# Performance work log

Measured on AMD Instinct MI355X. Metric: run time of the kernel, lower is better.

Reference implementation:

```python
import jax, jax.numpy as jnp
import numpy as np

N_PULSES = 8_000_000
NUM_DOMS = 200_000
EPS = 1e-08


def setup_inputs() -> dict:
    key = jax.random.key(0)
    k1, k2, k3 = jax.random.split(key, 3)
    times = jax.random.normal(k1, (N_PULSES,), dtype=jnp.float32) * 100.0
    charges = jax.random.uniform(k2, (N_PULSES,), dtype=jnp.float32) * 10.0
    dom_idx = jax.random.randint(k3, (N_PULSES,), 0, NUM_DOMS, dtype=jnp.int32)
    return {"times": times, "charges": charges, "dom_idx": dom_idx, "num_doms": NUM_DOMS}


def reference(times, charges, dom_idx, num_doms):
    n = times.shape[0]
    ones = jnp.ones_like(times)
    # per-DOM pulse counts (float, matching torch's float scatter_add of ones)
    count = jnp.zeros((num_doms,), dtype=times.dtype).at[dom_idx].add(ones)

    # --- temporal features ---
    first_times = jnp.full((num_doms,), jnp.inf, dtype=times.dtype).at[dom_idx].min(times)
    delta_t_first = times - first_times[dom_idx]

    mean_times = jnp.zeros((num_doms,), dtype=times.dtype).at[dom_idx].add(times) / (count + EPS)
    mean_e = mean_times[dom_idx]
    delta_t_median = times - mean_e

    var = jnp.zeros((num_doms,), dtype=times.dtype).at[dom_idx].add((times - mean_e) ** 2) / (count + EPS)
    time_std = jnp.sqrt(var + EPS)
    t_normalized = (times - mean_e) / (time_std[dom_idx] + EPS)

    # --- charge features ---
    total_charges = jnp.zeros((num_doms,), dtype=charges.dtype).at[dom_idx].add(charges)
    charge_fraction = charges / (total_charges[dom_idx] + EPS)

    max_charges = jnp.full((num_doms,), -jnp.inf, dtype=charges.dtype).at[dom_idx].max(charges)
    charge_ratio = charges / (max_charges[dom_idx] + EPS)

    # --- charge rank within each DOM (0 = brightest), fully vectorized ---
    # sort primarily by dom_idx, secondarily by descending charge
    order = jnp.lexsort((-charges, dom_idx))  # (n,)
    sorted_dom = dom_idx[order]
    counts_i = jnp.zeros((num_doms,), dtype=jnp.int32).at[dom_idx].add(jnp.ones_like(dom_idx))
    starts = jnp.cumsum(counts_i) - counts_i  # exclusive prefix-sum of group sizes
    rank_sorted = jnp.arange(n, dtype=jnp.int32) - starts[sorted_dom]
    ranks = jnp.zeros((n,), dtype=jnp.int32).at[order].set(rank_sorted)

    dom_sizes_e = count[dom_idx]  # float sizes per pulse
    log_charge_rank = jnp.log((ranks.astype(times.dtype) + 1.0) / (dom_sizes_e + EPS))

    return jnp.stack(
        [delta_t_first, delta_t_median, t_normalized,
         charge_fraction, charge_ratio, log_charge_rank], axis=1)
```

## Files before the change

### kernel.cpp

```cpp
#include <hip/hip_runtime.h>
#include <hip/hip_bf16.h>
#include <stdint.h>
#include <math.h>

#define NDOMS 200000
#define EPSF 1e-8f
#define DLBITS 8
#define DLMASK 255
#define NBUCK ((NDOMS + DLMASK) >> DLBITS)
#define NB2 (NBUCK * 2)
#define CAP_B 11264
#define CAP_H 6016
#define CSTRIDE 16
#define CHUNK 8192
#define IDXM 0x7FFFFFu

typedef unsigned long long u64;

__device__ __forceinline__ unsigned f2mono(float f){
  unsigned b = __float_as_uint(f);
  return b ^ (unsigned)(((int)b >> 31) | 0x80000000);
}
__device__ __forceinline__ float mono2f(unsigned u){
  unsigned b = (u & 0x80000000u) ? (u ^ 0x80000000u) : ~u;
  return __uint_as_float(b);
}

__global__ void k_init(int* __restrict__ gcursor){
  int i = blockIdx.x * blockDim.x + threadIdx.x;
  if (i < NB2) gcursor[i * CSTRIDE] = 0;
}

__global__ void __launch_bounds__(512)
k_bin(const float* __restrict__ charges, const int* __restrict__ dom,
      const float* __restrict__ times, int n, int* __restrict__ gcursor,
      uint4* __restrict__ rec_g){
  __shared__ int lhist[NB2];
  __shared__ int lbase[NB2];
  __shared__ int lcnt[NB2];
  int t = threadIdx.x;
  int start = blockIdx.x * CHUNK;
  int end = min(start + CHUNK, n);
  for (int i = t; i < NB2; i += 512) lhist[i] = 0;
  __syncthreads();
  for (int p = start + t; p < end; p += 512)
    atomicAdd(&lhist[dom[p] >> 7], 1);
  __syncthreads();
  for (int i = t; i < NB2; i += 512){
    int c = lhist[i];
    lbase[i] = c ? atomicAdd(&gcursor[i * CSTRIDE], c) : 0;
    lcnt[i] = 0;
  }
  __syncthreads();
  for (int p = start + t; p < end; p += 512){
    int d = dom[p];
    int i2 = d >> 7;
    int pos = lbase[i2] + atomicAdd(&lcnt[i2], 1);
    if (pos < CAP_B){
      int b = i2 >> 1;
      int slot = (i2 & 1) ? (CAP_B - 1 - pos) : pos;
      uint4 r;
      r.x = ((unsigned)(d & DLMASK) << 23) | (IDXM - (unsigned)p);
      r.y = __float_as_uint(charges[p]);
      r.z = __float_as_uint(times[p]);
      r.w = (unsigned)d;
      rec_g[(size_t)b * CAP_B + slot] = r;
    }
  }
}

__global__ void __launch_bounds__(512)
k_grp(const uint4* __restrict__ rec_g, const int* __restrict__ gcursor,
      float* __restrict__ derived, unsigned char* __restrict__ rank8p){
  __shared__ u64   keysL[CAP_H];
  __shared__ int hist[128], starts[128], cur[128];
  __shared__ float s_t[128], s_t2[128], s_c[128];
  __shared__ unsigned mn_t[128], mx_c[128];
  int bid = blockIdx.x, b = bid >> 1, h = bid & 1, t = threadIdx.x;
  int cl = min(gcursor[(2 * b) * CSTRIDE], CAP_B);
  int ch = min(gcursor[(2 * b + 1) * CSTRIDE], CAP_B - cl);
  int myCnt  = h ? ch : cl;
  if (myCnt > CAP_H) myCnt = CAP_H;
  int myBase = h ? (CAP_B - ch) : 0;
  const uint4* rg = rec_g + (size_t)b * CAP_B + myBase;

  if (t < 128){
    hist[t] = 0; s_t[t] = 0.f; s_t2[t] = 0.f; s_c[t] = 0.f;
    mn_t[t] = 0xFFFFFFFFu; mx_c[t] = 0u;
  }
  __syncthreads();
  unsigned rx[12], ry[12], rz[12];
  #pragma unroll
  for (int i = 0; i < 12; ++i){
    int s = t + i * 512;
    if (s < myCnt){
      uint4 r = rg[s];
      rx[i] = r.x; ry[i] = r.y; rz[i] = r.z;
      int dl = (int)((r.x >> 23) & 127);
      float tv = __uint_as_float(r.z);
      atomicAdd(&hist[dl], 1);
      atomicAdd(&s_t[dl], tv);
      atomicAdd(&s_t2[dl], tv * tv);
      atomicAdd(&s_c[dl], __uint_as_float(r.y));
      atomicMax(&mx_c[dl], r.y);
      atomicMin(&mn_t[dl], f2mono(tv));
    }
  }
  __syncthreads();
  if (t < 128) starts[t] = hist[t];
  __syncthreads();
  for (int off = 1; off < 128; off <<= 1){
    int v = 0;
    if (t < 128 && t >= off) v = starts[t - off];
    __syncthreads();
    if (t < 128) starts[t] += v;
    __syncthreads();
  }
  if (t < 128){ starts[t] -= hist[t]; cur[t] = starts[t]; }
  __syncthreads();
  #pragma unroll
  for (int i = 0; i < 12; ++i){
    int s = t + i * 512;
    if (s < myCnt){
      int dl = (int)((rx[i] >> 23) & 127);
      int pos = atomicAdd(&cur[dl], 1);
      keysL[pos] = ((u64)ry[i] << 32) | rx[i];
    }
  }
  __syncthreads();
  if (t < 128){
    int k = hist[t];
    if (k > 0){
      int d = b * 256 + h * 128 + t;
      float kf = (float)k;
      float m  = s_t[t] / (kf + EPSF);
      float var = (s_t2[t] - 2.0f * m * s_t[t] + kf * m * m) / (kf + EPSF);
      var = fmaxf(var, 0.0f);
      float* dv = derived + (size_t)d * 8;
      dv[0] = mono2f(mn_t[t]);
      dv[1] = m;
      dv[2] = 1.0f / (sqrtf(var + EPSF) + EPSF);
      dv[3] = 1.0f / (s_c[t] + EPSF);
      dv[4] = 1.0f / (__uint_as_float(mx_c[t]) + EPSF);
      dv[5] = kf; dv[6] = 0.f; dv[7] = 0.f;
    }
  }
  for (int s = t; s < myCnt; s += 512){
    u64 me = keysL[s];
    int dl = (int)((me >> 23) & 127);
    int st = starts[dl], k = hist[dl];
    int r = 0;
    for (int j = st; j < st + k; ++j) r += (keysL[j] > me) ? 1 : 0;
    rank8p[IDXM - (unsigned)(me & IDXM)] = (unsigned char)r;
  }
}

__global__ void __launch_bounds__(256)
k_out(const float* __restrict__ times, const float* __restrict__ charges,
      const int* __restrict__ dom, const unsigned char* __restrict__ rank8p,
      const float* __restrict__ derived, int n, float* __restrict__ out){
  __shared__ float st[1536];
  int b = blockIdx.x, t = threadIdx.x;
  int p = b * 256 + t;
  float f[6] = {0.f, 0.f, 0.f, 0.f, 0.f, 0.f};
  if (p < n){
    float tv = times[p], cv = charges[p];
    int d = dom[p];
    float r = (float)rank8p[p];
    const float4* dv = (const float4*)(derived + (size_t)d * 8);
    float4 d0 = dv[0];
    float4 d1 = dv[1];
    float dm = tv - d0.y;
    f[0] = tv - d0.x;
    f[1] = dm;
    f[2] = dm * d0.z;
    f[3] = cv * d0.w;
    f[4] = cv * d1.x;
    f[5] = logf((r + 1.0f) / (d1.y + EPSF));
  }
  if ((b + 1) * 256 <= n){
    #pragma unroll
    for (int j = 0; j < 6; ++j) st[t * 6 + j] = f[j];
    __syncthreads();
    float* ob = out + (size_t)b * 1536;
    #pragma unroll
    for (int j = 0; j < 6; ++j) ob[j * 256 + t] = st[j * 256 + t];
  } else if (p < n){
    for (int j = 0; j < 6; ++j) out[(size_t)p * 6 + j] = f[j];
  }
}

extern "C" void kernel_launch(void* const* d_in, const int* in_sizes, int n_in,
                              void* d_out, int out_size, void* d_ws, size_t ws_size,
                              hipStream_t stream) {
  const float* times   = (const float*)d_in[0];
  const float* charges = (const float*)d_in[1];
  const int*   dom     = (const int*)d_in[2];
  const int n = in_sizes[0];

  char* w = (char*)d_ws;
  int*   gcursor = (int*)w;   w += ((size_t)NB2 * CSTRIDE * 4 + 255) & ~255ull;
  float* derived = (float*)w; w += (size_t)NDOMS * 32;
  unsigned char* rank8p = (unsigned char*)w; w += (size_t)n;

  uint4* rec_g = (uint4*)d_out;

  k_init<<<(NB2 + 255) / 256, 256, 0, stream>>>(gcursor);
  k_bin<<<(n + CHUNK - 1) / CHUNK, 512, 0, stream>>>(charges, dom, times, n,
                                                     gcursor, rec_g);
  k_grp<<<NB2, 512, 0, stream>>>(rec_g, gcursor, derived, rank8p);
  k_out<<<(n + 255) / 256, 256, 0, stream>>>(times, charges, dom, rank8p,
                                             derived, n, (float*)d_out);
}
```

Measured before the change: 817.3 us.

## Write ranks to bucket-local slots and gather them back via a slot index

Rank writes in the grouping kernel used to scatter one byte per pulse to random global positions. Now each rank is written contiguously into a per-bucket array, indexed by the slot recorded during binning. A new gather kernel then reads each pulse's rank back in pulse order. This replaces random byte stores with coalesced ones, at the cost of an extra launch, a 2-byte slot index per pulse, and a random gather read.

```diff
diff --git a/kernel.cpp b/kernel.cpp
--- a/kernel.cpp
+++ b/kernel.cpp
@@ -34,7 +34,7 @@
 __global__ void __launch_bounds__(512)
 k_bin(const float* __restrict__ charges, const int* __restrict__ dom,
       const float* __restrict__ times, int n, int* __restrict__ gcursor,
-      uint4* __restrict__ rec_g){
+      uint4* __restrict__ rec_g, unsigned short* __restrict__ slotidx){
   __shared__ int lhist[NB2];
   __shared__ int lbase[NB2];
   __shared__ int lcnt[NB2];
@@ -65,14 +65,16 @@
       r.z = __float_as_uint(times[p]);
       r.w = (unsigned)d;
       rec_g[(size_t)b * CAP_B + slot] = r;
+      slotidx[p] = (unsigned short)slot;
     }
   }
 }
 
 __global__ void __launch_bounds__(512)
 k_grp(const uint4* __restrict__ rec_g, const int* __restrict__ gcursor,
-      float* __restrict__ derived, unsigned char* __restrict__ rank8p){
+      float* __restrict__ derived, unsigned char* __restrict__ rank_bkt){
   __shared__ u64   keysL[CAP_H];
+  __shared__ unsigned short slotS[CAP_H];
   __shared__ int hist[128], starts[128], cur[128];
   __shared__ float s_t[128], s_t2[128], s_c[128];
   __shared__ unsigned mn_t[128], mx_c[128];
@@ -125,6 +127,7 @@
       int dl = (int)((rx[i] >> 23) & 127);
       int pos = atomicAdd(&cur[dl], 1);
       keysL[pos] = ((u64)ry[i] << 32) | rx[i];
+      slotS[pos] = (unsigned short)s;
     }
   }
   __syncthreads();
@@ -145,13 +148,25 @@
       dv[5] = kf; dv[6] = 0.f; dv[7] = 0.f;
     }
   }
-  for (int s = t; s < myCnt; s += 512){
-    u64 me = keysL[s];
+  unsigned char* rb = rank_bkt + (size_t)b * CAP_B + myBase;
+  for (int q = t; q < myCnt; q += 512){
+    u64 me = keysL[q];
     int dl = (int)((me >> 23) & 127);
     int st = starts[dl], k = hist[dl];
     int r = 0;
     for (int j = st; j < st + k; ++j) r += (keysL[j] > me) ? 1 : 0;
-    rank8p[IDXM - (unsigned)(me & IDXM)] = (unsigned char)r;
+    rb[slotS[q]] = (unsigned char)r;
+  }
+}
+
+__global__ void __launch_bounds__(256)
+k_gat(const int* __restrict__ dom, const unsigned short* __restrict__ slotidx,
+      const unsigned char* __restrict__ rank_bkt, int n,
+      unsigned char* __restrict__ rank8){
+  int p = blockIdx.x * 256 + threadIdx.x;
+  if (p < n){
+    int b = dom[p] >> DLBITS;
+    rank8[p] = rank_bkt[(size_t)b * CAP_B + slotidx[p]];
   }
 }
 
@@ -201,14 +216,19 @@
   char* w = (char*)d_ws;
   int*   gcursor = (int*)w;   w += ((size_t)NB2 * CSTRIDE * 4 + 255) & ~255ull;
   float* derived = (float*)w; w += (size_t)NDOMS * 32;
-  unsigned char* rank8p = (unsigned char*)w; w += (size_t)n;
+  unsigned char* rank8 = (unsigned char*)w; w += (size_t)n;
 
   uint4* rec_g = (uint4*)d_out;
+  unsigned short* slotidx =
+      (unsigned short*)((char*)d_out + (size_t)NBUCK * CAP_B * 16);
+  unsigned char* rank_bkt =
+      (unsigned char*)((char*)d_out + (size_t)NBUCK * CAP_B * 16 + (size_t)2 * n);
 
   k_init<<<(NB2 + 255) / 256, 256, 0, stream>>>(gcursor);
   k_bin<<<(n + CHUNK - 1) / CHUNK, 512, 0, stream>>>(charges, dom, times, n,
-                                                     gcursor, rec_g);
-  k_grp<<<NB2, 512, 0, stream>>>(rec_g, gcursor, derived, rank8p);
-  k_out<<<(n + 255) / 256, 256, 0, stream>>>(times, charges, dom, rank8p,
+                                                     gcursor, rec_g, slotidx);
+  k_grp<<<NB2, 512, 0, stream>>>(rec_g, gcursor, derived, rank_bkt);
+  k_gat<<<(n + 255) / 256, 256, 0, stream>>>(dom, slotidx, rank_bkt, n, rank8);
+  k_out<<<(n + 255) / 256, 256, 0, stream>>>(times, charges, dom, rank8,
                                              derived, n, (float*)d_out);
 }
```

After: 869.7 us. +6.4%, slower.
